# Kernel tuning notes

Hardware: AMD Instinct MI355X
Metric: run time of the kernel (lower is better)

The kernel has to match this reference:

```python
import jax, jax.numpy as jnp
import numpy as np

HIDDEN = 1024
N_HEAD = 16
D_HEAD = HIDDEN // N_HEAD


def setup_inputs() -> dict:
    key = jax.random.key(0)
    ks = jax.random.split(key, 12)
    B, S, H = 2, 2048, HIDDEN
    scale = 1.0 / np.sqrt(H)
    inp = {
        "q": jax.random.normal(ks[0], (B, S, H), jnp.float32),
        "k": jax.random.normal(ks[1], (B, S, H), jnp.float32),
        "v": jax.random.normal(ks[2], (B, S, H), jnp.float32),
        "mask": jnp.ones((B, 1, S, S), jnp.int32),
        "w_q": jax.random.normal(ks[3], (H, H), jnp.float32) * scale,
        "b_q": jnp.zeros((H,), jnp.float32),
        "w_k": jax.random.normal(ks[4], (H, H), jnp.float32) * scale,
        "b_k": jnp.zeros((H,), jnp.float32),
        "w_v": jax.random.normal(ks[5], (H, H), jnp.float32) * scale,
        "b_v": jnp.zeros((H,), jnp.float32),
        "w_o": jax.random.normal(ks[6], (H, H), jnp.float32) * scale,
        "b_o": jnp.zeros((H,), jnp.float32),
    }
    return inp


def reference(q, k, v, mask, w_q, b_q, w_k, b_k, w_v, b_v, w_o, b_o):
    B, Sq, H = q.shape
    Sk = k.shape[1]
    # projections (weights stored as [in, out])
    qh = (q @ w_q + b_q).reshape(B, Sq, N_HEAD, D_HEAD).transpose(0, 2, 1, 3)
    kh = (k @ w_k + b_k).reshape(B, Sk, N_HEAD, D_HEAD).transpose(0, 2, 1, 3)
    vh = (v @ w_v + b_v).reshape(B, Sk, N_HEAD, D_HEAD).transpose(0, 2, 1, 3)
    scores = jnp.einsum("bhqd,bhkd->bhqk", qh, kh) * (D_HEAD ** -0.5)
    scores = jnp.where(mask == 0, jnp.float32(-10000.0), scores)
    attn = jax.nn.softmax(scores, axis=-1)
    out = jnp.einsum("bhqk,bhkd->bhqd", attn, vh)
    out = out.transpose(0, 2, 1, 3).reshape(B, Sq, H)
    return out @ w_o + b_o
```

## Files before the change

kernel.cpp:

```cpp
#include <hip/hip_runtime.h>
#include <hip/hip_bf16.h>
#include <stdint.h>

#define S_LEN 2048
#define HID   1024
#define NHEAD 16
#define DHEAD 64
#define BATCH 2

#define QSCALE 0.18033688f
#define MASKNEG -14427.0f

typedef __bf16 bf16_t;
typedef __bf16 bf16x4 __attribute__((ext_vector_type(4)));
typedef __bf16 bf16x8 __attribute__((ext_vector_type(8)));
typedef float  f32x4  __attribute__((ext_vector_type(4)));


__device__ __forceinline__ void gl_lds16(const bf16_t* g, bf16_t* l) {
  __builtin_amdgcn_global_load_lds((const __attribute__((address_space(1))) void*)g,
                                   (__attribute__((address_space(3))) void*)l,
                                   16, 0, 0);
}

template<int TR, int TC, int NW = 4>
__device__ __forceinline__ void stage_tile(const bf16_t* __restrict__ g, int ldg,
                                           bf16_t* lds, int wave, int lane) {
  constexpr int CH = TC / 8;
  constexpr int NINST = (TR * CH) / 64;
  #pragma unroll
  for (int i = wave; i < NINST; i += NW) {
    int slot = i * 64 + lane;
    int r  = slot / CH;
    int cs = slot & (CH - 1);
    int c  = cs ^ (r & (CH - 1));
    gl_lds16(g + (size_t)r * ldg + c * 8, lds + i * 512);
  }
}

template<int CH>
__device__ __forceinline__ bf16x8 frag_ld(const bf16_t* lds, int row, int kchunk) {
  int cs = kchunk ^ (row & (CH - 1));
  return *(const bf16x8*)(lds + (row * CH + cs) * 8);
}

__global__ __launch_bounds__(256) void cvt3(const float* __restrict__ q,
                                            const float* __restrict__ k,
                                            const float* __restrict__ v,
                                            bf16_t* __restrict__ qb,
                                            bf16_t* __restrict__ kb,
                                            bf16_t* __restrict__ vb) {
  int which = blockIdx.y;
  const float* src = which == 0 ? q : which == 1 ? k : v;
  bf16_t* dst = which == 0 ? qb : which == 1 ? kb : vb;
  size_t i = ((size_t)blockIdx.x * 256 + threadIdx.x) * 4;
  float4 u = *(const float4*)(src + i);
  bf16x4 o = {(bf16_t)u.x, (bf16_t)u.y, (bf16_t)u.z, (bf16_t)u.w};
  *(bf16x4*)(dst + i) = o;
}

__global__ __launch_bounds__(256) void transpose_w4(
    const float* __restrict__ w0, const float* __restrict__ w1,
    const float* __restrict__ w2, const float* __restrict__ w3,
    bf16_t* __restrict__ wt, int* __restrict__ flags) {
  if (blockIdx.x == 0 && blockIdx.y == 0 && blockIdx.z == 0) {
    flags[threadIdx.x] = -1;
    flags[threadIdx.x + 256] = -1;
  }
  __shared__ float t[64][65];
  const float* W = blockIdx.z == 0 ? w0 : blockIdx.z == 1 ? w1 : blockIdx.z == 2 ? w2 : w3;
  bf16_t* WT = wt + (size_t)blockIdx.z * HID * HID;
  int tx = threadIdx.x & 63, ty = threadIdx.x >> 6;
  int r0 = blockIdx.y * 64, c0 = blockIdx.x * 64;
  #pragma unroll
  for (int i = ty; i < 64; i += 4) t[i][tx] = W[(size_t)(r0 + i) * HID + c0 + tx];
  __syncthreads();
  #pragma unroll
  for (int i = ty; i < 64; i += 4) WT[(size_t)(c0 + i) * HID + r0 + tx] = (bf16_t)t[tx][i];
}

__global__ __launch_bounds__(256) void mask_flags(const int* __restrict__ mask,
                                                  int* __restrict__ flags) {
  int qtile = blockIdx.x, rg = blockIdx.y, b = blockIdx.z;
  const int* base = mask + (size_t)b * S_LEN * S_LEN
                  + (size_t)(qtile * 128 + rg * 16) * S_LEN;
  int tid = threadIdx.x;
  int kt = tid >> 4;
  int ok = 1;
  #pragma unroll
  for (int r = 0; r < 16; ++r) {
    const int4* p = (const int4*)(base + (size_t)r * S_LEN + tid * 8);
    int4 a = p[0], c = p[1];
    ok &= (a.x != 0) & (a.y != 0) & (a.z != 0) & (a.w != 0) &
          (c.x != 0) & (c.y != 0) & (c.z != 0) & (c.w != 0);
  }
  __shared__ int oks[16];
  if (tid < 16) oks[tid] = -1;
  __syncthreads();
  if (!ok) atomicAnd(&oks[kt], 0);
  __syncthreads();
  if (tid < 16 && oks[tid] == 0) atomicAnd(&flags[(b * 16 + qtile) * 16 + tid], 0);
}

__global__ __launch_bounds__(256) void qkv_gemm(
    const bf16_t* __restrict__ qb, const bf16_t* __restrict__ kb, const bf16_t* __restrict__ vb,
    const bf16_t* __restrict__ wT,
    const float* __restrict__ bq, const float* __restrict__ bk, const float* __restrict__ bv,
    bf16_t* __restrict__ Qh, bf16_t* __restrict__ Kh, bf16_t* __restrict__ VhT) {
  int mode = blockIdx.z;
  const bf16_t* A    = mode == 0 ? qb : mode == 1 ? kb : vb;
  const bf16_t* Bt   = wT + (size_t)mode * HID * HID;
  const float*  bias = mode == 0 ? bq : mode == 1 ? bk : bv;

  __shared__ __align__(16) bf16_t As[128 * 64];
  __shared__ __align__(16) bf16_t Bs[128 * 64];

  int tid = threadIdx.x, wave = tid >> 6, lane = tid & 63;
  int lane15 = lane & 15, quad = lane >> 4;
  int m0 = blockIdx.x * 128, n0 = blockIdx.y * 128;
  int wm = (wave >> 1) * 64, wn = (wave & 1) * 64;

  f32x4 zero4 = {0.f, 0.f, 0.f, 0.f};
  f32x4 acc[4][4];
  #pragma unroll
  for (int t = 0; t < 4; ++t)
    #pragma unroll
    for (int n = 0; n < 4; ++n) acc[t][n] = zero4;

  for (int k0 = 0; k0 < HID; k0 += 64) {
    stage_tile<128, 64>(A  + (size_t)m0 * HID + k0, HID, As, wave, lane);
    stage_tile<128, 64>(Bt + (size_t)n0 * HID + k0, HID, Bs, wave, lane);
    __syncthreads();
    #pragma unroll
    for (int kc = 0; kc < 2; ++kc) {
      bf16x8 af[4], bfr[4];
      #pragma unroll
      for (int t = 0; t < 4; ++t) af[t]  = frag_ld<8>(As, wm + t * 16 + lane15, kc * 4 + quad);
      #pragma unroll
      for (int n = 0; n < 4; ++n) bfr[n] = frag_ld<8>(Bs, wn + n * 16 + lane15, kc * 4 + quad);
      if (mode < 2) {
        #pragma unroll
        for (int t = 0; t < 4; ++t)
          #pragma unroll
          for (int n = 0; n < 4; ++n)
            acc[t][n] = __builtin_amdgcn_mfma_f32_16x16x32_bf16(af[t], bfr[n], acc[t][n], 0, 0, 0);
      } else {
        #pragma unroll
        for (int t = 0; t < 4; ++t)
          #pragma unroll
          for (int n = 0; n < 4; ++n)
            acc[t][n] = __builtin_amdgcn_mfma_f32_16x16x32_bf16(bfr[n], af[t], acc[t][n], 0, 0, 0);
      }
    }
    __syncthreads();
  }

  if (mode < 2) {
    float sc = (mode == 0) ? QSCALE : 1.0f;
    bf16_t* dst = (mode == 0 ? Qh : Kh);
    #pragma unroll
    for (int t = 0; t < 4; ++t) {
      #pragma unroll
      for (int n = 0; n < 4; ++n) {
        int col = n0 + wn + n * 16 + lane15;
        float bb = bias[col];
        #pragma unroll
        for (int i = 0; i < 4; ++i) {
          int row = m0 + wm + t * 16 + quad * 4 + i;
          bf16_t o = (bf16_t)((acc[t][n][i] + bb) * sc);
          int b = row >> 11, s = row & 2047;
          int h = col >> 6,  d = col & 63;
          dst[((size_t)(b * NHEAD + h) * S_LEN + s) * DHEAD + d] = o;
        }
      }
    }
  } else {
    #pragma unroll
    for (int n = 0; n < 4; ++n) {
      int dbase = n0 + wn + n * 16 + quad * 4;
      float4 bb4 = *(const float4*)(bias + dbase);
      #pragma unroll
      for (int t = 0; t < 4; ++t) {
        int token = m0 + wm + t * 16 + lane15;
        int b = token >> 11, s = token & 2047;
        #pragma unroll
        for (int i = 0; i < 4; ++i) {
          int dg = dbase + i;
          int h = dg >> 6, d = dg & 63;
          float bb = i == 0 ? bb4.x : i == 1 ? bb4.y : i == 2 ? bb4.z : bb4.w;
          VhT[((size_t)(b * NHEAD + h) * DHEAD + d) * S_LEN + s] = (bf16_t)(acc[t][n][i] + bb);
        }
      }
    }
  }
}

__global__ __launch_bounds__(512) void attn_kernel(
    const bf16_t* __restrict__ Qh, const bf16_t* __restrict__ Kh, const bf16_t* __restrict__ VhT,
    const int* __restrict__ mask, const int* __restrict__ flags,
    bf16_t* __restrict__ O) {
  __shared__ __align__(16) bf16_t Ks[2][64 * 64];
  __shared__ __align__(16) bf16_t VTs[2][80 * 64];
  __shared__ __align__(16) bf16_t Ps[128 * 64];

  int tid = threadIdx.x, wave = tid >> 6, lane = tid & 63;
  int lane15 = lane & 15, quad = lane >> 4;
  int bh = blockIdx.y, b = bh >> 4, h = bh & 15;
  int qt = blockIdx.x;
  int wrow = wave * 16;

  const bf16_t* Kbase = Kh + (size_t)bh * S_LEN * DHEAD;
  const bf16_t* Vbase = VhT + (size_t)bh * DHEAD * S_LEN;
  const int* flagrow = flags + (b * 16 + qt) * 16;

  if (tid < 64) {
    VTs[0][64 * 64 + tid] = (bf16_t)1.0f;
    VTs[1][64 * 64 + tid] = (bf16_t)1.0f;
  }

  stage_tile<128, 64, 8>(Qh + ((size_t)bh * S_LEN + qt * 128) * DHEAD, DHEAD, Ps, wave, lane);
  stage_tile<64, 64, 8>(Kbase, DHEAD, Ks[0], wave, lane);
  stage_tile<64, 64, 8>(Vbase, S_LEN, VTs[0], wave, lane);
  __syncthreads();

  bf16x8 qa[2];
  #pragma unroll
  for (int kc = 0; kc < 2; ++kc)
    qa[kc] = frag_ld<8>(Ps, wrow + lane15, kc * 4 + quad);

  f32x4 zero4 = {0.f, 0.f, 0.f, 0.f};
  f32x4 o_acc[5];
  #pragma unroll
  for (int mt = 0; mt < 5; ++mt) o_acc[mt] = zero4;

  int cur = 0;
  for (int kt = 0; kt < S_LEN / 64; ++kt) {
    if (kt + 1 < S_LEN / 64) {
      stage_tile<64, 64, 8>(Kbase + (size_t)(kt + 1) * 64 * DHEAD, DHEAD, Ks[cur ^ 1], wave, lane);
      stage_tile<64, 64, 8>(Vbase + (kt + 1) * 64, S_LEN, VTs[cur ^ 1], wave, lane);
    }
    const bf16_t* Kc = Ks[cur];
    const bf16_t* Vc = VTs[cur];

    f32x4 sa[4];
    {
      bf16x8 kf[4];
      #pragma unroll
      for (int mc = 0; mc < 4; ++mc) kf[mc] = frag_ld<8>(Kc, mc * 16 + lane15, quad);
      __builtin_amdgcn_s_setprio(1);
      #pragma unroll
      for (int mc = 0; mc < 4; ++mc)
        sa[mc] = __builtin_amdgcn_mfma_f32_16x16x32_bf16(kf[mc], qa[0], zero4, 0, 0, 0);
      __builtin_amdgcn_s_setprio(0);
      #pragma unroll
      for (int mc = 0; mc < 4; ++mc) kf[mc] = frag_ld<8>(Kc, mc * 16 + lane15, 4 + quad);
      __builtin_amdgcn_s_setprio(1);
      #pragma unroll
      for (int mc = 0; mc < 4; ++mc)
        sa[mc] = __builtin_amdgcn_mfma_f32_16x16x32_bf16(kf[mc], qa[1], sa[mc], 0, 0, 0);
      __builtin_amdgcn_s_setprio(0);
    }

    if (flagrow[kt >> 1] == 0) {
      int q = qt * 128 + wrow + lane15;
      #pragma unroll
      for (int mc = 0; mc < 4; ++mc)
        #pragma unroll
        for (int i = 0; i < 4; ++i) {
          int c = kt * 64 + mc * 16 + quad * 4 + i;
          if (mask[(size_t)b * S_LEN * S_LEN + (size_t)q * S_LEN + c] == 0)
            sa[mc][i] = MASKNEG;
        }
    }

    {
      int q = wrow + lane15;
      #pragma unroll
      for (int mc = 0; mc < 4; ++mc) {
        bf16x4 pk = {(bf16_t)exp2f(sa[mc][0]), (bf16_t)exp2f(sa[mc][1]),
                     (bf16_t)exp2f(sa[mc][2]), (bf16_t)exp2f(sa[mc][3])};
        int chunk = mc * 2 + (quad >> 1);
        int slot = chunk ^ (q & 7);
        *(bf16x4*)(Ps + q * 64 + slot * 8 + (quad & 1) * 4) = pk;
      }
    }

    #pragma unroll
    for (int kc = 0; kc < 2; ++kc) {
      bf16x8 vf[5], pf;
      #pragma unroll
      for (int mt = 0; mt < 5; ++mt) vf[mt] = frag_ld<8>(Vc, mt * 16 + lane15, kc * 4 + quad);
      pf = frag_ld<8>(Ps, wrow + lane15, kc * 4 + quad);
      __builtin_amdgcn_s_setprio(1);
      #pragma unroll
      for (int mt = 0; mt < 5; ++mt)
        o_acc[mt] = __builtin_amdgcn_mfma_f32_16x16x32_bf16(vf[mt], pf, o_acc[mt], 0, 0, 0);
      __builtin_amdgcn_s_setprio(0);
    }

    __syncthreads();
    cur ^= 1;
  }

  {
    float lval = __shfl(o_acc[4][0], lane15);
    float inv = 1.0f / lval;
    int s = qt * 128 + wrow + lane15;
    size_t orow = ((size_t)b * S_LEN + s) * HID + h * DHEAD;
    #pragma unroll
    for (int mt = 0; mt < 4; ++mt) {
      bf16x4 ov = {(bf16_t)(o_acc[mt][0] * inv), (bf16_t)(o_acc[mt][1] * inv),
                   (bf16_t)(o_acc[mt][2] * inv), (bf16_t)(o_acc[mt][3] * inv)};
      *(bf16x4*)(O + orow + mt * 16 + quad * 4) = ov;
    }
  }
}

__global__ __launch_bounds__(256) void oproj_gemm(
    const bf16_t* __restrict__ A, const bf16_t* __restrict__ Bt,
    const float* __restrict__ bias, float* __restrict__ out) {
  __shared__ __align__(16) bf16_t As[128 * 64];
  __shared__ __align__(16) bf16_t Bs[128 * 64];

  int tid = threadIdx.x, wave = tid >> 6, lane = tid & 63;
  int lane15 = lane & 15, quad = lane >> 4;
  int m0 = blockIdx.x * 128, n0 = blockIdx.y * 128;
  int wm = (wave >> 1) * 64, wn = (wave & 1) * 64;

  f32x4 zero4 = {0.f, 0.f, 0.f, 0.f};
  f32x4 acc[4][4];
  #pragma unroll
  for (int t = 0; t < 4; ++t)
    #pragma unroll
    for (int n = 0; n < 4; ++n) acc[t][n] = zero4;

  for (int k0 = 0; k0 < HID; k0 += 64) {
    stage_tile<128, 64>(A  + (size_t)m0 * HID + k0, HID, As, wave, lane);
    stage_tile<128, 64>(Bt + (size_t)n0 * HID + k0, HID, Bs, wave, lane);
    __syncthreads();
    #pragma unroll
    for (int kc = 0; kc < 2; ++kc) {
      bf16x8 af[4], bfr[4];
      #pragma unroll
      for (int t = 0; t < 4; ++t) af[t]  = frag_ld<8>(As, wm + t * 16 + lane15, kc * 4 + quad);
      #pragma unroll
      for (int n = 0; n < 4; ++n) bfr[n] = frag_ld<8>(Bs, wn + n * 16 + lane15, kc * 4 + quad);
      #pragma unroll
      for (int t = 0; t < 4; ++t)
        #pragma unroll
        for (int n = 0; n < 4; ++n)
          acc[t][n] = __builtin_amdgcn_mfma_f32_16x16x32_bf16(af[t], bfr[n], acc[t][n], 0, 0, 0);
    }
    __syncthreads();
  }

  #pragma unroll
  for (int t = 0; t < 4; ++t) {
    #pragma unroll
    for (int n = 0; n < 4; ++n) {
      int col = n0 + wn + n * 16 + lane15;
      float bb = bias[col];
      #pragma unroll
      for (int i = 0; i < 4; ++i) {
        int row = m0 + wm + t * 16 + quad * 4 + i;
        out[(size_t)row * HID + col] = acc[t][n][i] + bb;
      }
    }
  }
}

extern "C" void kernel_launch(void* const* d_in, const int* in_sizes, int n_in,
                              void* d_out, int out_size, void* d_ws, size_t ws_size,
                              hipStream_t stream) {
  (void)in_sizes; (void)n_in; (void)out_size; (void)ws_size;
  const float* q  = (const float*)d_in[0];
  const float* k  = (const float*)d_in[1];
  const float* v  = (const float*)d_in[2];
  const int*  mask = (const int*)d_in[3];
  const float* wq = (const float*)d_in[4];
  const float* bq = (const float*)d_in[5];
  const float* wk = (const float*)d_in[6];
  const float* bk = (const float*)d_in[7];
  const float* wv = (const float*)d_in[8];
  const float* bv = (const float*)d_in[9];
  const float* wo = (const float*)d_in[10];
  const float* bo = (const float*)d_in[11];

  char* ws = (char*)d_ws;
  bf16_t* wT    = (bf16_t*)(ws);
  bf16_t* Qh    = (bf16_t*)(ws + (8u  << 20));
  bf16_t* Kh    = (bf16_t*)(ws + (16u << 20));
  bf16_t* VhT   = (bf16_t*)(ws + (24u << 20));
  bf16_t* qb    = (bf16_t*)(ws + (32u << 20));
  bf16_t* kb    = (bf16_t*)(ws + (40u << 20));
  bf16_t* vb    = (bf16_t*)(ws + (48u << 20));
  int* flags    = (int*)(ws + (56u << 20));
  bf16_t* Obuf  = qb;

  cvt3<<<dim3(4096, 3), 256, 0, stream>>>(q, k, v, qb, kb, vb);
  transpose_w4<<<dim3(16, 16, 4), 256, 0, stream>>>(wq, wk, wv, wo, wT, flags);
  mask_flags<<<dim3(16, 8, 2), 256, 0, stream>>>(mask, flags);
  qkv_gemm<<<dim3(32, 8, 3), 256, 0, stream>>>(qb, kb, vb, wT, bq, bk, bv, Qh, Kh, VhT);
  attn_kernel<<<dim3(16, 32), 512, 0, stream>>>(Qh, Kh, VhT, mask, flags, Obuf);
  oproj_gemm<<<dim3(32, 8), 256, 0, stream>>>(Obuf, wT + (size_t)3 * HID * HID, bo, (float*)d_out);
}
```

Measured before the change: 272.4 us.

## Deepen attention K/V pipeline to four buffers with partial waitcnt and XCD-aware block mapping

Raises the attention kernel's K/V LDS staging from two to four buffers, prefetching two tiles ahead. A partial vmcnt wait plus a raw barrier at the top of each iteration replaces the full __syncthreads at the end, so global loads stay in flight across iterations. Blocks are remapped so that all query tiles of one (batch, head) land on the same XCD, which should improve L2 reuse of K/V. The per-tile flag reads are folded into a register bitmask, and the row-sum MFMA now takes a register constant of ones rather than an LDS row. The risks are more LDS use per block and the correctness of the hand-written wait counts.

```diff
diff --git a/kernel.cpp b/kernel.cpp
--- a/kernel.cpp
+++ b/kernel.cpp
@@ -199,48 +199,59 @@
     const bf16_t* __restrict__ Qh, const bf16_t* __restrict__ Kh, const bf16_t* __restrict__ VhT,
     const int* __restrict__ mask, const int* __restrict__ flags,
     bf16_t* __restrict__ O) {
-  __shared__ __align__(16) bf16_t Ks[2][64 * 64];
-  __shared__ __align__(16) bf16_t VTs[2][80 * 64];
+  __shared__ __align__(16) bf16_t Ks[4][64 * 64];
+  __shared__ __align__(16) bf16_t VTs[4][64 * 64];
   __shared__ __align__(16) bf16_t Ps[128 * 64];
 
   int tid = threadIdx.x, wave = tid >> 6, lane = tid & 63;
   int lane15 = lane & 15, quad = lane >> 4;
-  int bh = blockIdx.y, b = bh >> 4, h = bh & 15;
-  int qt = blockIdx.x;
-  int wrow = wave * 16;
+  int L = blockIdx.x + (blockIdx.y << 4);
+  int xcd = L & 7, slot = L >> 3;
+  int bh = xcd + ((slot >> 4) << 3);
+  int qt = slot & 15;
+  int b = bh >> 4, h = bh & 15;
+  int wrow = wave << 4;
 
   const bf16_t* Kbase = Kh + (size_t)bh * S_LEN * DHEAD;
   const bf16_t* Vbase = VhT + (size_t)bh * DHEAD * S_LEN;
   const int* flagrow = flags + (b * 16 + qt) * 16;
 
-  if (tid < 64) {
-    VTs[0][64 * 64 + tid] = (bf16_t)1.0f;
-    VTs[1][64 * 64 + tid] = (bf16_t)1.0f;
-  }
+  int fmask = 0;
+  #pragma unroll
+  for (int j = 0; j < 16; ++j) fmask |= (flagrow[j] == 0 ? 1 : 0) << j;
 
   stage_tile<128, 64, 8>(Qh + ((size_t)bh * S_LEN + qt * 128) * DHEAD, DHEAD, Ps, wave, lane);
   stage_tile<64, 64, 8>(Kbase, DHEAD, Ks[0], wave, lane);
   stage_tile<64, 64, 8>(Vbase, S_LEN, VTs[0], wave, lane);
-  __syncthreads();
+  stage_tile<64, 64, 8>(Kbase + (size_t)64 * DHEAD, DHEAD, Ks[1], wave, lane);
+  stage_tile<64, 64, 8>(Vbase + 64, S_LEN, VTs[1], wave, lane);
+  asm volatile("s_waitcnt vmcnt(4)" ::: "memory");
+  __builtin_amdgcn_s_barrier();
 
   bf16x8 qa[2];
   #pragma unroll
   for (int kc = 0; kc < 2; ++kc)
     qa[kc] = frag_ld<8>(Ps, wrow + lane15, kc * 4 + quad);
 
+  bf16x8 ones8;
+  #pragma unroll
+  for (int j = 0; j < 8; ++j) ones8[j] = (bf16_t)1.0f;
+
   f32x4 zero4 = {0.f, 0.f, 0.f, 0.f};
   f32x4 o_acc[5];
   #pragma unroll
   for (int mt = 0; mt < 5; ++mt) o_acc[mt] = zero4;
 
-  int cur = 0;
   for (int kt = 0; kt < S_LEN / 64; ++kt) {
-    if (kt + 1 < S_LEN / 64) {
-      stage_tile<64, 64, 8>(Kbase + (size_t)(kt + 1) * 64 * DHEAD, DHEAD, Ks[cur ^ 1], wave, lane);
-      stage_tile<64, 64, 8>(Vbase + (kt + 1) * 64, S_LEN, VTs[cur ^ 1], wave, lane);
-    }
-    const bf16_t* Kc = Ks[cur];
-    const bf16_t* Vc = VTs[cur];
+    int nt = kt + 2 <= 31 ? kt + 2 : 31;
+    int nbuf = (kt + 2) & 3;
+    stage_tile<64, 64, 8>(Kbase + (size_t)nt * 64 * DHEAD, DHEAD, Ks[nbuf], wave, lane);
+    stage_tile<64, 64, 8>(Vbase + nt * 64, S_LEN, VTs[nbuf], wave, lane);
+    asm volatile("s_waitcnt vmcnt(4)" ::: "memory");
+    __builtin_amdgcn_s_barrier();
+
+    const bf16_t* Kc = Ks[kt & 3];
+    const bf16_t* Vc = VTs[kt & 3];
 
     f32x4 sa[4];
     {
@@ -261,7 +272,7 @@
       __builtin_amdgcn_s_setprio(0);
     }
 
-    if (flagrow[kt >> 1] == 0) {
+    if ((fmask >> (kt >> 1)) & 1) {
       int q = qt * 128 + wrow + lane15;
       #pragma unroll
       for (int mc = 0; mc < 4; ++mc)
@@ -287,19 +298,17 @@
 
     #pragma unroll
     for (int kc = 0; kc < 2; ++kc) {
-      bf16x8 vf[5], pf;
-      #pragma unroll
-      for (int mt = 0; mt < 5; ++mt) vf[mt] = frag_ld<8>(Vc, mt * 16 + lane15, kc * 4 + quad);
+      bf16x8 vf[4], pf;
+      #pragma unroll
+      for (int mt = 0; mt < 4; ++mt) vf[mt] = frag_ld<8>(Vc, mt * 16 + lane15, kc * 4 + quad);
       pf = frag_ld<8>(Ps, wrow + lane15, kc * 4 + quad);
       __builtin_amdgcn_s_setprio(1);
       #pragma unroll
-      for (int mt = 0; mt < 5; ++mt)
+      for (int mt = 0; mt < 4; ++mt)
         o_acc[mt] = __builtin_amdgcn_mfma_f32_16x16x32_bf16(vf[mt], pf, o_acc[mt], 0, 0, 0);
+      o_acc[4] = __builtin_amdgcn_mfma_f32_16x16x32_bf16(ones8, pf, o_acc[4], 0, 0, 0);
       __builtin_amdgcn_s_setprio(0);
     }
-
-    __syncthreads();
-    cur ^= 1;
   }
 
   {
```

Result: no change. 270.2 us (-0.8%).
